# Kernel tuning notes

Measured on AMD Instinct MI355X. Metric: run time of the kernel, lower is better.

The kernel has to match this reference:

```python
import jax, jax.numpy as jnp
import numpy as np

N = 50000       # nodes
E = 1600000     # edges (before self-loops)
DIN = 128       # input_dim
HID = 32        # hidden_dim per head
H = 4           # num_heads
HD = HID * H    # 128, concat-head width
DOUT = 128      # output_dim
NC = 2          # num_classes
G = 256         # graphs in batch
NEG_SLOPE = 0.2
BN_EPS = 1e-5


def setup_inputs() -> dict:
    key = jax.random.key(0)
    ks = jax.random.split(key, 20)
    p = lambda k, shp: (jax.random.normal(k, shp, jnp.float32) * 0.05)
    x = jax.random.normal(ks[0], (N, DIN), jnp.float32)
    edge_index = jax.random.randint(ks[1], (2, E), 0, N, dtype=jnp.int32)
    batch = jnp.sort(jax.random.randint(ks[2], (N,), 0, G, dtype=jnp.int32))
    return {
        "x": x, "edge_index": edge_index, "batch": batch,
        # GATConv 1: lin weight [DIN, H*HID], att vectors [H, HID], bias [H*HID]
        "W1": p(ks[3], (DIN, HD)), "a1_src": p(ks[4], (H, HID)), "a1_dst": p(ks[5], (H, HID)), "b1": p(ks[6], (HD,)),
        "bn1_g": jnp.ones((HD,), jnp.float32), "bn1_b": jnp.zeros((HD,), jnp.float32),
        # GATConv 2: in = H*HID
        "W2": p(ks[7], (HD, HD)), "a2_src": p(ks[8], (H, HID)), "a2_dst": p(ks[9], (H, HID)), "b2": p(ks[10], (HD,)),
        "bn2_g": jnp.ones((HD,), jnp.float32), "bn2_b": jnp.zeros((HD,), jnp.float32),
        "L1W": p(ks[11], (HD, DOUT)), "L1b": p(ks[12], (DOUT,)),
        "L2W": p(ks[13], (DOUT, NC)), "L2b": p(ks[14], (NC,)),
    }


def _add_self_loops(edge_index, n):
    loops = jnp.arange(n, dtype=edge_index.dtype)
    return jnp.concatenate([edge_index, jnp.stack([loops, loops])], axis=1)


def _gat_conv(x, edge_index, W, a_src, a_dst, bias):
    # PyG GATConv: h = x @ W -> [N,H,F]; per-edge score = LeakyReLU(a_src.h_src + a_dst.h_dst);
    # softmax over incoming edges of each dst node; weighted scatter-add; concat heads + bias.
    n = x.shape[0]
    h = (x @ W).reshape(n, H, HID)
    src, dst = edge_index[0], edge_index[1]
    alpha_s = jnp.sum(h * a_src[None], axis=-1)   # [N,H]
    alpha_d = jnp.sum(h * a_dst[None], axis=-1)   # [N,H]
    e = jax.nn.leaky_relu(alpha_s[src] + alpha_d[dst], NEG_SLOPE)  # [E,H]
    m = jax.ops.segment_max(e, dst, num_segments=n)                # stable softmax over neighbors
    ex = jnp.exp(e - m[dst])
    s = jax.ops.segment_sum(ex, dst, num_segments=n)
    alpha = ex / (s[dst] + 1e-16)                                  # [E,H]
    out = jax.ops.segment_sum(h[src] * alpha[:, :, None], dst, num_segments=n)  # [N,H,F]
    return out.reshape(n, H * HID) + bias


def _batch_norm(x, gamma, beta):
    mu = jnp.mean(x, axis=0)
    var = jnp.mean((x - mu) ** 2, axis=0)
    return gamma * (x - mu) * jax.lax.rsqrt(var + BN_EPS) + beta


def reference(x, edge_index, batch, W1, a1_src, a1_dst, b1, bn1_g, bn1_b,
              W2, a2_src, a2_dst, b2, bn2_g, bn2_b, L1W, L1b, L2W, L2b):
    ei = _add_self_loops(edge_index, x.shape[0])
    h = jax.nn.relu(_gat_conv(x, ei, W1, a1_src, a1_dst, b1))
    h = _batch_norm(h, bn1_g, bn1_b)
    h = jax.nn.relu(_gat_conv(h, ei, W2, a2_src, a2_dst, b2))
    h = _batch_norm(h, bn2_g, bn2_b)
    # global mean pool over graph ids
    sums = jax.ops.segment_sum(h, batch, num_segments=G)
    cnts = jax.ops.segment_sum(jnp.ones((h.shape[0],), h.dtype), batch, num_segments=G)
    pooled = sums / jnp.maximum(cnts, 1.0)[:, None]   # [G, HD]
    z = jax.nn.relu(pooled @ L1W + L1b)               # dropout inactive at eval
    return z @ L2W + L2b                              # [G, NC]
```

## Files before the change

### kernel.cpp

```cpp
#include <hip/hip_runtime.h>
#include <math.h>

#define NN 50000
#define EE 1600000
#define GG 256
#define PAD 80
#define NB 256
#define EPB 6250
#define NR 8
#define RNG 6250
#define BCAP 960
#define NSH 16

constexpr float NEG = 0.2f;
constexpr float BN_EPS = 1e-5f;

typedef __attribute__((ext_vector_type(8))) short short8;
typedef __attribute__((ext_vector_type(4))) float f32x4;

constexpr int PB_W1 = 0, PB_A1S = 16384, PB_A1D = 16512, PB_B1 = 16640,
              PB_G1 = 16768, PB_BE1 = 16896, PB_W2 = 17024, PB_A2S = 33408,
              PB_A2D = 33536, PB_B2 = 33664, PB_G2 = 33792, PB_BE2 = 33920,
              PB_L1W = 34048, PB_L1B = 50432, PB_L2W = 50560, PB_L2B = 50816,
              PB_TOTAL = 50818;

struct PtrPack { const void* p[16]; };

__device__ __forceinline__ float b2f(unsigned short u) {
  unsigned v = ((unsigned)u) << 16;
  float f;
  __builtin_memcpy(&f, &v, 4);
  return f;
}
__device__ __forceinline__ float b2f_lo(unsigned u) {
  unsigned v = u << 16;
  float f;
  __builtin_memcpy(&f, &v, 4);
  return f;
}
__device__ __forceinline__ float b2f_hi(unsigned u) {
  unsigned v = u & 0xffff0000u;
  float f;
  __builtin_memcpy(&f, &v, 4);
  return f;
}
__device__ __forceinline__ unsigned short f2b(float f) {
  unsigned x;
  __builtin_memcpy(&x, &f, 4);
  unsigned r = x + 0x7FFFu + ((x >> 16) & 1u);
  return (unsigned short)(r >> 16);
}

__global__ __launch_bounds__(256) void k_prep(PtrPack pk, const unsigned short* __restrict__ xb,
                                              const int* __restrict__ batch,
                                              const int* __restrict__ esrc,
                                              const int* __restrict__ edst,
                                              int* __restrict__ flag,
                                              float* __restrict__ pb,
                                              int* __restrict__ starts, float* __restrict__ bnacc,
                                              int* __restrict__ ctrs,
                                              unsigned char* __restrict__ hist,
                                              unsigned* __restrict__ buck, int* __restrict__ bcnt,
                                              unsigned short* __restrict__ Wt1,
                                              float* __restrict__ wzero,
                                              float* __restrict__ poolsum) {
  const int segoff[17] = {0, 16384, 16512, 16640, 16768, 16896, 17024, 33408,
                          33536, 33664, 33792, 33920, 34048, 50432, 50560, 50816, 50818};
  __shared__ unsigned hcnt[25000];
  __shared__ int bc[NR];
  __shared__ int cs;
  int c = blockIdx.x, t = threadIdx.x;
  if (t == 0) cs = 0;
  if (t < NR) bc[t] = 0;
  for (int j = t; j < 25000; j += 256) hcnt[j] = 0u;
  __syncthreads();
  int sane = 0;
  for (int i = t; i < 4096; i += 256) {
    float a = fabsf(b2f(xb[i]));
    if (a > 1e-4f && a < 100.f) sane++;
  }
  atomicAdd(&cs, sane);
  int e0 = c * EPB;
  for (int i = t; i < EPB; i += 256) {
    int e = e0 + i;
    int d = edst[e];
    if ((unsigned)d >= (unsigned)NN) continue;
    int s = esrc[e];
    if ((unsigned)s >= (unsigned)NN) s = 0;
    int sh = (d & 1) * 16;
    unsigned old = atomicAdd(&hcnt[d >> 1], 1u << sh);
    unsigned rank = (old >> sh) & 0xFFFFu;
    if (rank > 7u) continue;
    int r = d / RNG;
    int dl = d - r * RNG;
    int pos = atomicAdd(&bc[r], 1);
    if (pos < BCAP)
      buck[(c * NR + r) * BCAP + pos] = ((unsigned)s << 16) | ((unsigned)dl << 3) | rank;
  }
  __syncthreads();
  int bf = (cs > 3482) ? 1 : 0;
  if (c == 0 && t == 0) *flag = bf;
  if (t < NR) bcnt[c * NR + t] = min(bc[t], BCAP);
  for (int j = t; j < NN; j += 256) {
    unsigned cc = (hcnt[j >> 1] >> ((j & 1) * 16)) & 0xFFFFu;
    hist[c * NN + j] = (unsigned char)min(cc, 255u);
  }
  for (int j = t; j < 199; j += 256) {
    int i = c * 199 + j;
    if (i < PB_TOTAL) {
      int seg = 0;
      while (i >= segoff[seg + 1]) seg++;
      int k = i - segoff[seg];
      pb[i] = bf ? b2f(((const unsigned short*)pk.p[seg])[k]) : ((const float*)pk.p[seg])[k];
    }
  }
  for (int j = t; j < 64; j += 256) {
    int i = c * 64 + j;
    int n = i & 127, k = i >> 7;
    Wt1[n * 128 + k] = bf ? ((const unsigned short*)pk.p[0])[k * 128 + n]
                          : f2b(((const float*)pk.p[0])[k * 128 + n]);
  }
  for (int j = t; j < 128; j += 256) poolsum[c * 128 + j] = 0.f;
  if (t < 32) bnacc[c * 32 + t] = 0.f;
  for (int j = t; j < 196; j += 256) {
    int n = c * 196 + j;
    if (n < NN) {
      int bb = batch[n];
      bb = min(max(bb, 0), GG - 1);
      int bp = (n == 0) ? -1 : batch[n - 1];
      bp = min(max(bp, -1), GG - 1);
      for (int gg = bp + 1; gg <= bb; gg++) starts[gg] = n;
      if (n == NN - 1)
        for (int gg = bb + 1; gg <= GG; gg++) starts[gg] = NN;
    }
  }
  if (c == 255 && t < 8) ctrs[t] = 0;
}

__global__ __launch_bounds__(256) void k_base(const unsigned char* __restrict__ hist,
                                              unsigned char* __restrict__ base,
                                              int* __restrict__ cnt) {
  int d = blockIdx.x * 256 + threadIdx.x;
  if (d >= NN) return;
  int run = 0;
  for (int b = 0; b < NB; b++) {
    int h = hist[b * NN + d];
    base[b * NN + d] = (unsigned char)min(run, 255);
    run += h;
  }
  cnt[d] = run;
}

__device__ __forceinline__ void gemm_body(float* cst, int bid,
                                          const unsigned short* __restrict__ Xb,
                                          const float* __restrict__ Xf, int bfm,
                                          const unsigned short* __restrict__ Wt,
                                          const float* __restrict__ shiftW,
                                          const float* __restrict__ aS,
                                          const float* __restrict__ aD,
                                          unsigned short* __restrict__ Y,
                                          float* __restrict__ as_, float* __restrict__ ad_) {
  int t = threadIdx.x;
  int row0 = bid * 64;
  int w = t >> 6, lane = t & 63;
  int m = lane & 15, quad = lane >> 4;
  int rA = min(row0 + w * 16 + m, NN - 1);
  short8 a4[4];
  if (bfm) {
    const short8* xp = (const short8*)(Xb + rA * 128);
#pragma unroll
    for (int kk = 0; kk < 4; kk++) a4[kk] = xp[kk * 4 + quad];
  } else {
#pragma unroll
    for (int kk = 0; kk < 4; kk++) {
      const float* xf = Xf + rA * 128 + kk * 32 + quad * 8;
#pragma unroll
      for (int j = 0; j < 8; j++) a4[kk][j] = (short)f2b(xf[j]);
    }
  }
  f32x4 acc[8] = {};
#pragma unroll
  for (int kk = 0; kk < 4; kk++) {
    int ko = kk * 32 + quad * 8;
#pragma unroll
    for (int n0 = 0; n0 < 8; n0++) {
      short8 b = *(const short8*)(Wt + (n0 * 16 + m) * 128 + ko);
      acc[n0] = __builtin_amdgcn_mfma_f32_16x16x32_bf16(a4[kk], b, acc[n0], 0, 0, 0);
    }
  }
#pragma unroll
  for (int n0 = 0; n0 < 8; n0++)
#pragma unroll
    for (int r = 0; r < 4; r++)
      cst[(w * 16 + quad * 4 + r) * 130 + n0 * 16 + m] = acc[n0][r];
  __syncthreads();
  int cg = t & 31, rg = t >> 5;
  int c0 = cg * 4;
  float a_s[4], a_d[4], sw[4];
#pragma unroll
  for (int j = 0; j < 4; j++) {
    a_s[j] = aS[c0 + j];
    a_d[j] = aD[c0 + j];
    sw[j] = shiftW[c0 + j];
  }
#pragma unroll
  for (int i = 0; i < 8; i++) {
    int rl = rg + i * 8;
    int row = row0 + rl;
    float v0 = cst[rl * 130 + c0 + 0] + sw[0];
    float v1 = cst[rl * 130 + c0 + 1] + sw[1];
    float v2 = cst[rl * 130 + c0 + 2] + sw[2];
    float v3 = cst[rl * 130 + c0 + 3] + sw[3];
    if (row < NN) {
      uint2 pk2;
      pk2.x = (unsigned)f2b(v0) | ((unsigned)f2b(v1) << 16);
      pk2.y = (unsigned)f2b(v2) | ((unsigned)f2b(v3) << 16);
      *reinterpret_cast<uint2*>(&Y[row * 128 + c0]) = pk2;
    }
    float ps = v0 * a_s[0] + v1 * a_s[1] + v2 * a_s[2] + v3 * a_s[3];
    float pd = v0 * a_d[0] + v1 * a_d[1] + v2 * a_d[2] + v3 * a_d[3];
    ps += __shfl_xor(ps, 1); ps += __shfl_xor(ps, 2); ps += __shfl_xor(ps, 4);
    pd += __shfl_xor(pd, 1); pd += __shfl_xor(pd, 2); pd += __shfl_xor(pd, 4);
    if ((cg & 7) == 0 && row < NN) {
      int hh = cg >> 3;
      as_[row * 4 + hh] = ps;
      ad_[row * 4 + hh] = pd;
    }
  }
}

__global__ __launch_bounds__(256) void k_fillgemm(const unsigned* __restrict__ buck,
                                                  const int* __restrict__ bcnt,
                                                  const unsigned char* __restrict__ base,
                                                  unsigned short* __restrict__ adj,
                                                  const unsigned short* __restrict__ Xb,
                                                  const float* __restrict__ Xf,
                                                  const int* __restrict__ flagp,
                                                  const unsigned short* __restrict__ Wt,
                                                  const float* __restrict__ shiftW,
                                                  const float* __restrict__ aS,
                                                  const float* __restrict__ aD,
                                                  unsigned short* __restrict__ Y,
                                                  float* __restrict__ as_, float* __restrict__ ad_) {
  __shared__ float cst[64 * 130];
  int idx = blockIdx.x;
  int t = threadIdx.x;
  if (idx < NB) {
    int r = idx & 7, g = idx >> 3;
    int dbase = r * RNG;
#pragma unroll 1
    for (int j = 0; j < 8; j++) {
      int c = g * 8 + j;
      int n = bcnt[c * NR + r];
      const unsigned* bk = buck + (c * NR + r) * BCAP;
      const unsigned char* bs = base + c * NN;
      for (int i = t; i < n; i += 256) {
        unsigned p = bk[i];
        int s = p >> 16;
        int dl = (p >> 3) & 0x1FFF;
        int rank = p & 7;
        int d = dbase + dl;
        int slot = (int)bs[d] + rank;
        if (slot < PAD) adj[d * PAD + slot] = (unsigned short)s;
      }
    }
  } else {
    gemm_body(cst, idx - NB, Xb, Xf, *flagp, Wt, shiftW, aS, aD, Y, as_, ad_);
  }
}

__global__ __launch_bounds__(256) void k_gemm(const unsigned short* __restrict__ Xb,
                                              const unsigned short* __restrict__ Wt,
                                              const float* __restrict__ shiftW,
                                              const float* __restrict__ aS,
                                              const float* __restrict__ aD,
                                              unsigned short* __restrict__ Y,
                                              float* __restrict__ as_, float* __restrict__ ad_) {
  __shared__ float cst[64 * 130];
  gemm_body(cst, blockIdx.x, Xb, nullptr, 1, Wt, shiftW, aS, aD, Y, as_, ad_);
}

__global__ __launch_bounds__(128) void k_agg(const unsigned short* __restrict__ adj,
                                             const int* __restrict__ cnt,
                                             const float4* __restrict__ asrc4,
                                             const float4* __restrict__ adst4,
                                             const uint4* __restrict__ hin4,
                                             const float* __restrict__ bias,
                                             unsigned short* __restrict__ out) {
  int n = blockIdx.x;
  int t = threadIdx.x;
  int deg = cnt[n];
  if (deg < 0) deg = 0;
  if (deg > PAD - 1) deg = PAD - 1;
  int tot = deg + 1;
  int beg = n * PAD;
  __shared__ float w[4][PAD];
  __shared__ int srcs[PAD];
  __shared__ float redv[8][128];
  __shared__ float lsw[2][4];
  float4 ad4 = adst4[n];
  float ls0 = 0.f, ls1 = 0.f, ls2 = 0.f, ls3 = 0.f;
  int g = t >> 4, L = t & 15, hd = L >> 2;
  float acc[8] = {};
  if (t < tot) {
    int s = (t < deg) ? (int)adj[beg + t] : n;
    if ((unsigned)s >= (unsigned)NN) s = n;
    float4 a = asrc4[s];
    float s0 = a.x + ad4.x; s0 = s0 > 0.f ? s0 : NEG * s0;
    float s1 = a.y + ad4.y; s1 = s1 > 0.f ? s1 : NEG * s1;
    float s2 = a.z + ad4.z; s2 = s2 > 0.f ? s2 : NEG * s2;
    float s3 = a.w + ad4.w; s3 = s3 > 0.f ? s3 : NEG * s3;
    ls0 = __expf(s0); ls1 = __expf(s1); ls2 = __expf(s2); ls3 = __expf(s3);
    w[0][t] = ls0; w[1][t] = ls1; w[2][t] = ls2; w[3][t] = ls3;
    srcs[t] = s;
  }
  __syncthreads();
  int e = g;
  for (; e + 24 < tot; e += 32) {
    float w1 = w[hd][e], w2 = w[hd][e + 8], w3 = w[hd][e + 16], w4 = w[hd][e + 24];
    int s1 = srcs[e], s2 = srcs[e + 8], s3 = srcs[e + 16], s4 = srcs[e + 24];
    uint4 v1 = hin4[s1 * 16 + L];
    uint4 v2 = hin4[s2 * 16 + L];
    uint4 v3 = hin4[s3 * 16 + L];
    uint4 v4 = hin4[s4 * 16 + L];
    acc[0] += w1 * b2f_lo(v1.x); acc[1] += w1 * b2f_hi(v1.x);
    acc[2] += w1 * b2f_lo(v1.y); acc[3] += w1 * b2f_hi(v1.y);
    acc[4] += w1 * b2f_lo(v1.z); acc[5] += w1 * b2f_hi(v1.z);
    acc[6] += w1 * b2f_lo(v1.w); acc[7] += w1 * b2f_hi(v1.w);
    acc[0] += w2 * b2f_lo(v2.x); acc[1] += w2 * b2f_hi(v2.x);
    acc[2] += w2 * b2f_lo(v2.y); acc[3] += w2 * b2f_hi(v2.y);
    acc[4] += w2 * b2f_lo(v2.z); acc[5] += w2 * b2f_hi(v2.z);
    acc[6] += w2 * b2f_lo(v2.w); acc[7] += w2 * b2f_hi(v2.w);
    acc[0] += w3 * b2f_lo(v3.x); acc[1] += w3 * b2f_hi(v3.x);
    acc[2] += w3 * b2f_lo(v3.y); acc[3] += w3 * b2f_hi(v3.y);
    acc[4] += w3 * b2f_lo(v3.z); acc[5] += w3 * b2f_hi(v3.z);
    acc[6] += w3 * b2f_lo(v3.w); acc[7] += w3 * b2f_hi(v3.w);
    acc[0] += w4 * b2f_lo(v4.x); acc[1] += w4 * b2f_hi(v4.x);
    acc[2] += w4 * b2f_lo(v4.y); acc[3] += w4 * b2f_hi(v4.y);
    acc[4] += w4 * b2f_lo(v4.z); acc[5] += w4 * b2f_hi(v4.z);
    acc[6] += w4 * b2f_lo(v4.w); acc[7] += w4 * b2f_hi(v4.w);
  }
  for (; e < tot; e += 8) {
    float wv = w[hd][e];
    int s = srcs[e];
    uint4 v = hin4[s * 16 + L];
    acc[0] += wv * b2f_lo(v.x); acc[1] += wv * b2f_hi(v.x);
    acc[2] += wv * b2f_lo(v.y); acc[3] += wv * b2f_hi(v.y);
    acc[4] += wv * b2f_lo(v.z); acc[5] += wv * b2f_hi(v.z);
    acc[6] += wv * b2f_lo(v.w); acc[7] += wv * b2f_hi(v.w);
  }
#pragma unroll
  for (int mm = 1; mm < 64; mm <<= 1) {
    ls0 += __shfl_xor(ls0, mm);
    ls1 += __shfl_xor(ls1, mm);
    ls2 += __shfl_xor(ls2, mm);
    ls3 += __shfl_xor(ls3, mm);
  }
  if ((t & 63) == 0) {
    int wv = t >> 6;
    lsw[wv][0] = ls0; lsw[wv][1] = ls1; lsw[wv][2] = ls2; lsw[wv][3] = ls3;
  }
#pragma unroll
  for (int j = 0; j < 8; j++) redv[g][8 * L + j] = acc[j];
  __syncthreads();
  float den = lsw[0][t >> 5] + lsw[1][t >> 5];
  float sum = 0.f;
#pragma unroll
  for (int g2 = 0; g2 < 8; g2++) sum += redv[g2][t];
  float o = sum / (den + 1e-16f) + bias[t];
  out[n * 128 + t] = f2b(o > 0.f ? o : 0.f);
}

__global__ __launch_bounds__(128) void k_bnstats(const unsigned* __restrict__ x32,
                                                 float* __restrict__ accum, int* __restrict__ ctr,
                                                 const float* __restrict__ g, const float* __restrict__ b,
                                                 float* __restrict__ scale, float* __restrict__ shift,
                                                 const float* __restrict__ W2f, float* __restrict__ sw2,
                                                 unsigned short* __restrict__ Wt2,
                                                 const int* __restrict__ batch,
                                                 float* __restrict__ poolsum) {
  __shared__ int lastflag;
  __shared__ float shs[128];
  __shared__ float scs[128];
  int t = threadIdx.x;
  int c2 = t & 63, half = t >> 6;
  int sh = blockIdx.x & (NSH - 1);
  int r0 = blockIdx.x * 196;
  int r1 = min(r0 + 196, NN);
  float s0 = 0.f, q0 = 0.f, s1 = 0.f, q1 = 0.f;
  if (poolsum) {
    int curg = -1;
    float p0 = 0.f, p1 = 0.f;
    for (int r = r0 + half; r < r1; r += 2) {
      int gg = batch[r];
      gg = min(max(gg, 0), GG - 1);
      if (gg != curg) {
        if (curg >= 0) {
          atomicAdd(&poolsum[curg * 128 + 2 * c2], p0);
          atomicAdd(&poolsum[curg * 128 + 2 * c2 + 1], p1);
        }
        curg = gg; p0 = 0.f; p1 = 0.f;
      }
      unsigned v = x32[r * 64 + c2];
      float lo = b2f_lo(v), hi = b2f_hi(v);
      s0 += lo; q0 += lo * lo; p0 += lo;
      s1 += hi; q1 += hi * hi; p1 += hi;
    }
    if (curg >= 0) {
      atomicAdd(&poolsum[curg * 128 + 2 * c2], p0);
      atomicAdd(&poolsum[curg * 128 + 2 * c2 + 1], p1);
    }
  } else {
    for (int r = r0 + half; r < r1; r += 2) {
      unsigned v = x32[r * 64 + c2];
      float lo = b2f_lo(v), hi = b2f_hi(v);
      s0 += lo; q0 += lo * lo;
      s1 += hi; q1 += hi * hi;
    }
  }
  float* ac = accum + sh * 256;
  atomicAdd(&ac[2 * c2], s0);
  atomicAdd(&ac[2 * c2 + 1], s1);
  atomicAdd(&ac[128 + 2 * c2], q0);
  atomicAdd(&ac[128 + 2 * c2 + 1], q1);
  __threadfence();
  if (t == 0) {
    int done = atomicAdd(ctr, 1);
    lastflag = (done == (int)gridDim.x - 1) ? 1 : 0;
  }
  __syncthreads();
  if (lastflag) {
    float ss = 0.f, qq = 0.f;
#pragma unroll
    for (int s2 = 0; s2 < NSH; s2++) {
      ss += atomicAdd(&accum[s2 * 256 + t], 0.f);
      qq += atomicAdd(&accum[s2 * 256 + 128 + t], 0.f);
    }
    float inv = 1.0f / NN;
    float mu = ss * inv;
    float var = qq * inv - mu * mu;
    float rs = rsqrtf(var + BN_EPS);
    float sc = g[t] * rs;
    float shv = b[t] - mu * sc;
    scale[t] = sc;
    shift[t] = shv;
    shs[t] = shv;
    scs[t] = sc;
    __syncthreads();
    if (W2f) {
      float s = 0.f;
      for (int k = 0; k < 128; k++) s += shs[k] * W2f[k * 128 + t];
      sw2[t] = s;
      for (int i = t; i < 16384; i += 128) {
        int n = i & 127, k = i >> 7;
        Wt2[n * 128 + k] = f2b(scs[k] * W2f[k * 128 + n]);
      }
    }
  }
}

__global__ __launch_bounds__(128) void k_head(const float* __restrict__ poolsum,
                                              const int* __restrict__ starts,
                                              const float* __restrict__ scale, const float* __restrict__ shift,
                                              const float* __restrict__ L1W, const float* __restrict__ L1b,
                                              const float* __restrict__ L2W, const float* __restrict__ L2b,
                                              const int* __restrict__ flagp, void* __restrict__ outp) {
  int g = blockIdx.x, t = threadIdx.x;
  int b0 = starts[g], b1 = starts[g + 1];
  b0 = min(max(b0, 0), NN);
  b1 = min(max(b1, 0), NN);
  int cnt = b1 - b0;
  __shared__ float pooled[128];
  float s = poolsum[g * 128 + t];
  pooled[t] = (cnt > 0) ? (s / cnt) * scale[t] + shift[t] : 0.f;
  __syncthreads();
  float z = L1b[t];
  for (int k = 0; k < 128; k++) z += pooled[k] * L1W[k * 128 + t];
  z = z > 0.f ? z : 0.f;
  __shared__ float r0a[128], r1a[128];
  r0a[t] = z * L2W[t * 2 + 0];
  r1a[t] = z * L2W[t * 2 + 1];
  __syncthreads();
  for (int d = 64; d >= 1; d >>= 1) {
    if (t < d) {
      r0a[t] += r0a[t + d];
      r1a[t] += r1a[t + d];
    }
    __syncthreads();
  }
  if (t == 0) {
    float o0 = r0a[0] + L2b[0];
    float o1 = r1a[0] + L2b[1];
    if (*flagp) {
      unsigned short* ob = (unsigned short*)outp;
      ob[g * 2 + 0] = f2b(o0);
      ob[g * 2 + 1] = f2b(o1);
    } else {
      float* of = (float*)outp;
      of[g * 2 + 0] = o0;
      of[g * 2 + 1] = o1;
    }
  }
}

extern "C" void kernel_launch(void* const* d_in, const int* in_sizes, int n_in,
                              void* d_out, int out_size, void* d_ws, size_t ws_size,
                              hipStream_t stream) {
  (void)in_sizes; (void)n_in; (void)out_size; (void)ws_size;
  const int* ei = (const int*)d_in[1];
  const int* batch = (const int*)d_in[2];

  float* ws = (float*)d_ws;
  size_t o = 0;
  int* flag = (int*)(ws + o);   o += 16;
  int* ctrs = (int*)(ws + o);   o += 16;
  float* pb = ws + o;           o += 51200;
  float* bnacc = ws + o;        o += 8192;
  float* scale1 = ws + o;       o += 128;
  float* shift1 = ws + o;       o += 128;
  float* scale2 = ws + o;       o += 128;
  float* shift2 = ws + o;       o += 128;
  float* wzero = ws + o;        o += 128;
  float* sw2 = ws + o;          o += 128;
  unsigned short* Wt1 = (unsigned short*)(ws + o); o += 8192;
  unsigned short* Wt2 = (unsigned short*)(ws + o); o += 8192;
  float* poolsum = ws + o;      o += GG * 128;
  int* cnt = (int*)(ws + o);    o += 50016;
  int* starts = (int*)(ws + o); o += 512;
  int* bcnt = (int*)(ws + o);   o += 2048;
  float* asrc = ws + o;         o += 200000;
  float* adst = ws + o;         o += 200000;
  unsigned* buck = (unsigned*)(ws + o);            o += NB * NR * BCAP;
  unsigned short* adj = (unsigned short*)(ws + o); o += NN * PAD / 2;
  unsigned short* hA = (unsigned short*)(ws + o);  o += 3200000;
  unsigned short* hB = (unsigned short*)(ws + o);  o += 3200000;

  unsigned char* hist = (unsigned char*)hB;
  unsigned char* base = (unsigned char*)hA;

  const int* esrc = ei;
  const int* edst = ei + EE;

  PtrPack pk;
  for (int i = 0; i < 16; i++) pk.p[i] = d_in[3 + i];

  k_prep<<<NB, 256, 0, stream>>>(pk, (const unsigned short*)d_in[0], batch, esrc, edst,
                                 flag, pb, starts, bnacc, ctrs, hist, buck, bcnt,
                                 Wt1, wzero, poolsum);
  k_base<<<196, 256, 0, stream>>>(hist, base, cnt);

  k_fillgemm<<<NB + 782, 256, 0, stream>>>(buck, bcnt, base, adj,
                                           (const unsigned short*)d_in[0], (const float*)d_in[0],
                                           flag, Wt1, wzero,
                                           pb + PB_A1S, pb + PB_A1D, hB, asrc, adst);
  k_agg<<<NN, 128, 0, stream>>>(adj, cnt, (const float4*)asrc, (const float4*)adst,
                                (const uint4*)hB, pb + PB_B1, hA);
  k_bnstats<<<256, 128, 0, stream>>>((const unsigned*)hA, bnacc, ctrs + 1,
                                     pb + PB_G1, pb + PB_BE1, scale1, shift1,
                                     pb + PB_W2, sw2, Wt2, nullptr, nullptr);

  k_gemm<<<782, 256, 0, stream>>>(hA, Wt2, sw2, pb + PB_A2S, pb + PB_A2D, hB, asrc, adst);
  k_agg<<<NN, 128, 0, stream>>>(adj, cnt, (const float4*)asrc, (const float4*)adst,
                                (const uint4*)hB, pb + PB_B2, hA);
  k_bnstats<<<256, 128, 0, stream>>>((const unsigned*)hA, bnacc + 4096, ctrs + 2,
                                     pb + PB_G2, pb + PB_BE2, scale2, shift2,
                                     nullptr, nullptr, nullptr, batch, poolsum);

  k_head<<<GG, 128, 0, stream>>>(poolsum, starts, scale2, shift2,
                                 pb + PB_L1W, pb + PB_L1B,
                                 pb + PB_L2W, pb + PB_L2B, flag, d_out);
}
```

Measured before the change: 416.8 us.

## Map one wavefront per node in aggregation with packed FMA and shuffle reduction

The aggregation kernel now processes four destination nodes per 256-thread block, one per wavefront, instead of one node per 128-thread block. Cross-group reductions use wave shuffles in place of shared memory and block barriers, and the bf16-times-weight accumulation uses v_pk_fma_f32 inline asm. The goal is to cut block-launch overhead, idle threads, and __syncthreads costs in the memory-bound gather. The trade-off is that each wave now walks its node's edges with 4 groups instead of 8, so per-node serial work roughly doubles.

```diff
diff --git a/kernel.cpp b/kernel.cpp
--- a/kernel.cpp
+++ b/kernel.cpp
@@ -17,6 +17,7 @@
 
 typedef __attribute__((ext_vector_type(8))) short short8;
 typedef __attribute__((ext_vector_type(4))) float f32x4;
+typedef __attribute__((ext_vector_type(2))) float f32x2;
 
 constexpr int PB_W1 = 0, PB_A1S = 16384, PB_A1D = 16512, PB_B1 = 16640,
               PB_G1 = 16768, PB_BE1 = 16896, PB_W2 = 17024, PB_A2S = 33408,
@@ -49,6 +50,11 @@
   __builtin_memcpy(&x, &f, 4);
   unsigned r = x + 0x7FFFu + ((x >> 16) & 1u);
   return (unsigned short)(r >> 16);
+}
+
+__device__ __forceinline__ void pkfma(f32x2& acc, unsigned u, f32x2 wp) {
+  f32x2 p = {b2f_lo(u), b2f_hi(u)};
+  asm("v_pk_fma_f32 %0, %1, %2, %0" : "+v"(acc) : "v"(p), "v"(wp));
 }
 
 __global__ __launch_bounds__(256) void k_prep(PtrPack pk, const unsigned short* __restrict__ xb,
@@ -280,74 +286,76 @@
   gemm_body(cst, blockIdx.x, Xb, nullptr, 1, Wt, shiftW, aS, aD, Y, as_, ad_);
 }
 
-__global__ __launch_bounds__(128) void k_agg(const unsigned short* __restrict__ adj,
+__global__ __launch_bounds__(256) void k_agg(const unsigned short* __restrict__ adj,
                                              const int* __restrict__ cnt,
                                              const float4* __restrict__ asrc4,
                                              const float4* __restrict__ adst4,
                                              const uint4* __restrict__ hin4,
                                              const float* __restrict__ bias,
                                              unsigned short* __restrict__ out) {
-  int n = blockIdx.x;
+  __shared__ float wq[4][PAD][4];
+  __shared__ int ws[4][PAD];
   int t = threadIdx.x;
+  int wid = t >> 6, lane = t & 63;
+  int n = blockIdx.x * 4 + wid;
   int deg = cnt[n];
   if (deg < 0) deg = 0;
   if (deg > PAD - 1) deg = PAD - 1;
   int tot = deg + 1;
   int beg = n * PAD;
-  __shared__ float w[4][PAD];
-  __shared__ int srcs[PAD];
-  __shared__ float redv[8][128];
-  __shared__ float lsw[2][4];
   float4 ad4 = adst4[n];
   float ls0 = 0.f, ls1 = 0.f, ls2 = 0.f, ls3 = 0.f;
-  int g = t >> 4, L = t & 15, hd = L >> 2;
-  float acc[8] = {};
-  if (t < tot) {
-    int s = (t < deg) ? (int)adj[beg + t] : n;
+  for (int b = lane; b < tot; b += 64) {
+    int s = (b < deg) ? (int)adj[beg + b] : n;
     if ((unsigned)s >= (unsigned)NN) s = n;
     float4 a = asrc4[s];
     float s0 = a.x + ad4.x; s0 = s0 > 0.f ? s0 : NEG * s0;
     float s1 = a.y + ad4.y; s1 = s1 > 0.f ? s1 : NEG * s1;
     float s2 = a.z + ad4.z; s2 = s2 > 0.f ? s2 : NEG * s2;
     float s3 = a.w + ad4.w; s3 = s3 > 0.f ? s3 : NEG * s3;
-    ls0 = __expf(s0); ls1 = __expf(s1); ls2 = __expf(s2); ls3 = __expf(s3);
-    w[0][t] = ls0; w[1][t] = ls1; w[2][t] = ls2; w[3][t] = ls3;
-    srcs[t] = s;
-  }
-  __syncthreads();
+    float e0 = __expf(s0), e1 = __expf(s1), e2 = __expf(s2), e3 = __expf(s3);
+    ls0 += e0; ls1 += e1; ls2 += e2; ls3 += e3;
+    *reinterpret_cast<float4*>(&wq[wid][b][0]) = make_float4(e0, e1, e2, e3);
+    ws[wid][b] = s;
+  }
+  asm volatile("" ::: "memory");
+  __builtin_amdgcn_wave_barrier();
+  int g = lane >> 4, L = lane & 15, hd = L >> 2;
+  const float (*wrow)[4] = wq[wid];
+  const int* srow = ws[wid];
+  f32x2 acc2[4] = {};
   int e = g;
-  for (; e + 24 < tot; e += 32) {
-    float w1 = w[hd][e], w2 = w[hd][e + 8], w3 = w[hd][e + 16], w4 = w[hd][e + 24];
-    int s1 = srcs[e], s2 = srcs[e + 8], s3 = srcs[e + 16], s4 = srcs[e + 24];
+  for (; e + 12 < tot; e += 16) {
+    float w1 = wrow[e][hd], w2 = wrow[e + 4][hd], w3 = wrow[e + 8][hd], w4 = wrow[e + 12][hd];
+    int s1 = srow[e], s2 = srow[e + 4], s3 = srow[e + 8], s4 = srow[e + 12];
     uint4 v1 = hin4[s1 * 16 + L];
     uint4 v2 = hin4[s2 * 16 + L];
     uint4 v3 = hin4[s3 * 16 + L];
     uint4 v4 = hin4[s4 * 16 + L];
-    acc[0] += w1 * b2f_lo(v1.x); acc[1] += w1 * b2f_hi(v1.x);
-    acc[2] += w1 * b2f_lo(v1.y); acc[3] += w1 * b2f_hi(v1.y);
-    acc[4] += w1 * b2f_lo(v1.z); acc[5] += w1 * b2f_hi(v1.z);
-    acc[6] += w1 * b2f_lo(v1.w); acc[7] += w1 * b2f_hi(v1.w);
-    acc[0] += w2 * b2f_lo(v2.x); acc[1] += w2 * b2f_hi(v2.x);
-    acc[2] += w2 * b2f_lo(v2.y); acc[3] += w2 * b2f_hi(v2.y);
-    acc[4] += w2 * b2f_lo(v2.z); acc[5] += w2 * b2f_hi(v2.z);
-    acc[6] += w2 * b2f_lo(v2.w); acc[7] += w2 * b2f_hi(v2.w);
-    acc[0] += w3 * b2f_lo(v3.x); acc[1] += w3 * b2f_hi(v3.x);
-    acc[2] += w3 * b2f_lo(v3.y); acc[3] += w3 * b2f_hi(v3.y);
-    acc[4] += w3 * b2f_lo(v3.z); acc[5] += w3 * b2f_hi(v3.z);
-    acc[6] += w3 * b2f_lo(v3.w); acc[7] += w3 * b2f_hi(v3.w);
-    acc[0] += w4 * b2f_lo(v4.x); acc[1] += w4 * b2f_hi(v4.x);
-    acc[2] += w4 * b2f_lo(v4.y); acc[3] += w4 * b2f_hi(v4.y);
-    acc[4] += w4 * b2f_lo(v4.z); acc[5] += w4 * b2f_hi(v4.z);
-    acc[6] += w4 * b2f_lo(v4.w); acc[7] += w4 * b2f_hi(v4.w);
-  }
-  for (; e < tot; e += 8) {
-    float wv = w[hd][e];
-    int s = srcs[e];
+    f32x2 p1 = {w1, w1}, p2 = {w2, w2}, p3 = {w3, w3}, p4 = {w4, w4};
+    pkfma(acc2[0], v1.x, p1); pkfma(acc2[1], v1.y, p1);
+    pkfma(acc2[2], v1.z, p1); pkfma(acc2[3], v1.w, p1);
+    pkfma(acc2[0], v2.x, p2); pkfma(acc2[1], v2.y, p2);
+    pkfma(acc2[2], v2.z, p2); pkfma(acc2[3], v2.w, p2);
+    pkfma(acc2[0], v3.x, p3); pkfma(acc2[1], v3.y, p3);
+    pkfma(acc2[2], v3.z, p3); pkfma(acc2[3], v3.w, p3);
+    pkfma(acc2[0], v4.x, p4); pkfma(acc2[1], v4.y, p4);
+    pkfma(acc2[2], v4.z, p4); pkfma(acc2[3], v4.w, p4);
+  }
+  for (; e < tot; e += 4) {
+    float wv = wrow[e][hd];
+    int s = srow[e];
     uint4 v = hin4[s * 16 + L];
-    acc[0] += wv * b2f_lo(v.x); acc[1] += wv * b2f_hi(v.x);
-    acc[2] += wv * b2f_lo(v.y); acc[3] += wv * b2f_hi(v.y);
-    acc[4] += wv * b2f_lo(v.z); acc[5] += wv * b2f_hi(v.z);
-    acc[6] += wv * b2f_lo(v.w); acc[7] += wv * b2f_hi(v.w);
+    f32x2 p = {wv, wv};
+    pkfma(acc2[0], v.x, p); pkfma(acc2[1], v.y, p);
+    pkfma(acc2[2], v.z, p); pkfma(acc2[3], v.w, p);
+  }
+#pragma unroll
+  for (int j = 0; j < 4; j++) {
+    acc2[j].x += __shfl_xor(acc2[j].x, 16);
+    acc2[j].y += __shfl_xor(acc2[j].y, 16);
+    acc2[j].x += __shfl_xor(acc2[j].x, 32);
+    acc2[j].y += __shfl_xor(acc2[j].y, 32);
   }
 #pragma unroll
   for (int mm = 1; mm < 64; mm <<= 1) {
@@ -356,19 +364,34 @@
     ls2 += __shfl_xor(ls2, mm);
     ls3 += __shfl_xor(ls3, mm);
   }
-  if ((t & 63) == 0) {
-    int wv = t >> 6;
-    lsw[wv][0] = ls0; lsw[wv][1] = ls1; lsw[wv][2] = ls2; lsw[wv][3] = ls3;
-  }
-#pragma unroll
-  for (int j = 0; j < 8; j++) redv[g][8 * L + j] = acc[j];
-  __syncthreads();
-  float den = lsw[0][t >> 5] + lsw[1][t >> 5];
-  float sum = 0.f;
-#pragma unroll
-  for (int g2 = 0; g2 < 8; g2++) sum += redv[g2][t];
-  float o = sum / (den + 1e-16f) + bias[t];
-  out[n * 128 + t] = f2b(o > 0.f ? o : 0.f);
+  if (g == 0) {
+    float den = (hd == 0) ? ls0 : (hd == 1) ? ls1 : (hd == 2) ? ls2 : ls3;
+    float inv = 1.0f / (den + 1e-16f);
+    const float4* bp = reinterpret_cast<const float4*>(bias + L * 8);
+    float4 b0 = bp[0], b1 = bp[1];
+    float o0 = acc2[0].x * inv + b0.x;
+    float o1 = acc2[0].y * inv + b0.y;
+    float o2 = acc2[1].x * inv + b0.z;
+    float o3 = acc2[1].y * inv + b0.w;
+    float o4 = acc2[2].x * inv + b1.x;
+    float o5 = acc2[2].y * inv + b1.y;
+    float o6 = acc2[3].x * inv + b1.z;
+    float o7 = acc2[3].y * inv + b1.w;
+    o0 = o0 > 0.f ? o0 : 0.f;
+    o1 = o1 > 0.f ? o1 : 0.f;
+    o2 = o2 > 0.f ? o2 : 0.f;
+    o3 = o3 > 0.f ? o3 : 0.f;
+    o4 = o4 > 0.f ? o4 : 0.f;
+    o5 = o5 > 0.f ? o5 : 0.f;
+    o6 = o6 > 0.f ? o6 : 0.f;
+    o7 = o7 > 0.f ? o7 : 0.f;
+    uint4 pk4;
+    pk4.x = (unsigned)f2b(o0) | ((unsigned)f2b(o1) << 16);
+    pk4.y = (unsigned)f2b(o2) | ((unsigned)f2b(o3) << 16);
+    pk4.z = (unsigned)f2b(o4) | ((unsigned)f2b(o5) << 16);
+    pk4.w = (unsigned)f2b(o6) | ((unsigned)f2b(o7) << 16);
+    *reinterpret_cast<uint4*>(&out[n * 128 + L * 8]) = pk4;
+  }
 }
 
 __global__ __launch_bounds__(128) void k_bnstats(const unsigned* __restrict__ x32,
@@ -553,15 +576,15 @@
                                            (const unsigned short*)d_in[0], (const float*)d_in[0],
                                            flag, Wt1, wzero,
                                            pb + PB_A1S, pb + PB_A1D, hB, asrc, adst);
-  k_agg<<<NN, 128, 0, stream>>>(adj, cnt, (const float4*)asrc, (const float4*)adst,
-                                (const uint4*)hB, pb + PB_B1, hA);
+  k_agg<<<NN / 4, 256, 0, stream>>>(adj, cnt, (const float4*)asrc, (const float4*)adst,
+                                    (const uint4*)hB, pb + PB_B1, hA);
   k_bnstats<<<256, 128, 0, stream>>>((const unsigned*)hA, bnacc, ctrs + 1,
                                      pb + PB_G1, pb + PB_BE1, scale1, shift1,
                                      pb + PB_W2, sw2, Wt2, nullptr, nullptr);
 
   k_gemm<<<782, 256, 0, stream>>>(hA, Wt2, sw2, pb + PB_A2S, pb + PB_A2D, hB, asrc, adst);
-  k_agg<<<NN, 128, 0, stream>>>(adj, cnt, (const float4*)asrc, (const float4*)adst,
-                                (const uint4*)hB, pb + PB_B2, hA);
+  k_agg<<<NN / 4, 256, 0, stream>>>(adj, cnt, (const float4*)asrc, (const float4*)adst,
+                                    (const uint4*)hB, pb + PB_B2, hA);
   k_bnstats<<<256, 128, 0, stream>>>((const unsigned*)hA, bnacc + 4096, ctrs + 2,
                                      pb + PB_G2, pb + PB_BE2, scale2, shift2,
                                      nullptr, nullptr, nullptr, batch, poolsum);
```

After: 408.7 us. No clear change (-1.9%).
